# Kernel optimization log

Measured on AMD Instinct MI355X. Metric: run time of the kernel, lower is better.

The kernel has to match this reference:

```python
import jax, jax.numpy as jnp
import numpy as np

EPS = 0.1        # entropic regularization epsilon
MAX_ITER = 15    # fixed number of Sinkhorn iterations (no early stop for determinism)
TINY = 1e-16     # denominator stabilizer, matches torch code
NORM_EPS = 1e-8  # cosine-norm clamp, matches torch code


def setup_inputs() -> dict:
    key = jax.random.key(0)
    k1, k2 = jax.random.split(key)
    x = jax.random.normal(k1, (32, 512, 256), dtype=jnp.float32)
    y = jax.random.normal(k2, (32, 512, 256), dtype=jnp.float32)
    return {"x": x, "y": y}


def _cosine_distance(x, y):
    # C[b,n,m] = 1 - <x_n, y_m> / max(|x_n||y_m|, eps)
    w1 = jnp.linalg.norm(x, axis=-1, keepdims=True)            # [b,n,1]
    w2 = jnp.linalg.norm(y, axis=-1, keepdims=True)            # [b,m,1]
    dots = jnp.einsum('bnd,bmd->bnm', x, y)                    # [b,n,m]
    denom = jnp.maximum(w1 * jnp.swapaxes(w2, -2, -1), NORM_EPS)
    return 1.0 - dots / denom


def _sinkhorn(C):
    nb, n, m = C.shape
    # uniform marginals (a=None, b=None in the torch module); mask is all ones
    a = jnp.full((nb, n), 1.0 / n, dtype=C.dtype)
    b = jnp.full((nb, m), 1.0 / m, dtype=C.dtype)

    def log_K(alpha, beta):
        # log K = (-C + alpha 1^T + 1 beta^T) / eps
        return (-C + alpha[:, :, None] + beta[:, None, :]) / EPS

    def step(carry, _):
        u, v, alpha, beta = carry
        K = jnp.exp(log_K(alpha, beta))
        u = a / (jnp.einsum('bnm,bm->bn', K, v) + TINY)   # K v
        v = b / (jnp.einsum('bnm,bn->bm', K, u) + TINY)   # K^T u
        alpha = alpha + EPS * jnp.log(u)  # absorb u into log scaling
        beta = beta + EPS * jnp.log(v)    # absorb v into log scaling
        return (u, v, alpha, beta), None

    init = (jnp.ones((nb, n), C.dtype), jnp.ones((nb, m), C.dtype),
            jnp.zeros((nb, n), C.dtype), jnp.zeros((nb, m), C.dtype))
    (u, v, alpha, beta), _ = jax.lax.scan(step, init, None, length=MAX_ITER)

    # P = exp(log u + log K + log v) with the FINAL alpha/beta (as in torch code)
    pi = jnp.exp(jnp.log(u)[:, :, None] + log_K(alpha, beta) + jnp.log(v)[:, None, :])
    cost = jnp.sum(pi * C, axis=(-2, -1))  # reduction='none' -> per-batch cost [nb]
    return cost, pi, C


def reference(x, y):
    C = _cosine_distance(x, y)
    return _sinkhorn(C)
```

## Files before the change

### kernel.cpp

```cpp
#include <hip/hip_runtime.h>
#include <hip/hip_fp16.h>
#include <math.h>

#define NB 32
#define NN 512
#define DD 256

constexpr float INV_EPS   = 10.0f;
constexpr float F_TINY    = 1e-16f;
constexpr float F_NORMEPS = 1e-8f;
constexpr float MARG      = 1.0f / 512.0f;

#define BARS_N 2048

typedef __attribute__((ext_vector_type(8))) short bf16x8;
typedef __attribute__((ext_vector_type(4))) float f32x4;

__device__ __forceinline__ unsigned short f2bf(float f) {
    unsigned u = __float_as_uint(f);
    u += 0x7fffu + ((u >> 16) & 1u);
    return (unsigned short)(u >> 16);
}
__device__ __forceinline__ int pack2(float a, float b) {
    return (int)f2bf(a) | ((int)f2bf(b) << 16);
}

__global__ __launch_bounds__(256) void gemm_cos_mfma(
        const float* __restrict__ x, const float* __restrict__ y,
        float* __restrict__ C, float* __restrict__ cost,
        int* __restrict__ bars) {
    int blk = blockIdx.x;
    int b = blk >> 4, ti = (blk >> 2) & 3, tj = blk & 3;
    if (blk == 0) {
        if (threadIdx.x < NB) cost[threadIdx.x] = 0.0f;
        for (int i = threadIdx.x; i < BARS_N; i += 256) bars[i] = 0;
    }
    __shared__ short Ah[128][32], Bh[128][32];
    __shared__ float sNx[128], sNy[128];
    const float* xb = x + ((size_t)b * NN + ti * 128) * DD;
    const float* yb = y + ((size_t)b * NN + tj * 128) * DD;
    int t = threadIdx.x, w = t >> 6, l = t & 63;
    int rw = w * 32, q = l >> 4, low = l & 15;

    f32x4 acc[2][8];
#pragma unroll
    for (int i = 0; i < 2; ++i)
#pragma unroll
        for (int j = 0; j < 8; ++j) acc[i][j] = (f32x4){0.f, 0.f, 0.f, 0.f};

    int sr = t >> 1, h = t & 1;
    int c0i = 2 * h, c1i = 2 * h + 1;
    int sw0 = (c0i ^ ((sr >> 1) & 3)) * 8;
    int sw1 = (c1i ^ ((sr >> 1) & 3)) * 8;
    float ssA = 0.0f, ssB = 0.0f;

    for (int k0 = 0; k0 < DD; k0 += 32) {
        {
            const float4* ga = (const float4*)(xb + (size_t)sr * DD + k0 + 16 * h);
            const float4* gc = (const float4*)(yb + (size_t)sr * DD + k0 + 16 * h);
            float4 a0 = ga[0], a1 = ga[1], a2 = ga[2], a3 = ga[3];
            float4 c0 = gc[0], c1 = gc[1], c2 = gc[2], c3 = gc[3];
            ssA += a0.x*a0.x + a0.y*a0.y + a0.z*a0.z + a0.w*a0.w;
            ssA += a1.x*a1.x + a1.y*a1.y + a1.z*a1.z + a1.w*a1.w;
            ssA += a2.x*a2.x + a2.y*a2.y + a2.z*a2.z + a2.w*a2.w;
            ssA += a3.x*a3.x + a3.y*a3.y + a3.z*a3.z + a3.w*a3.w;
            ssB += c0.x*c0.x + c0.y*c0.y + c0.z*c0.z + c0.w*c0.w;
            ssB += c1.x*c1.x + c1.y*c1.y + c1.z*c1.z + c1.w*c1.w;
            ssB += c2.x*c2.x + c2.y*c2.y + c2.z*c2.z + c2.w*c2.w;
            ssB += c3.x*c3.x + c3.y*c3.y + c3.z*c3.z + c3.w*c3.w;
            int4 pa0 = { pack2(a0.x,a0.y), pack2(a0.z,a0.w),
                         pack2(a1.x,a1.y), pack2(a1.z,a1.w) };
            int4 pa1 = { pack2(a2.x,a2.y), pack2(a2.z,a2.w),
                         pack2(a3.x,a3.y), pack2(a3.z,a3.w) };
            int4 pc0 = { pack2(c0.x,c0.y), pack2(c0.z,c0.w),
                         pack2(c1.x,c1.y), pack2(c1.z,c1.w) };
            int4 pc1 = { pack2(c2.x,c2.y), pack2(c2.z,c2.w),
                         pack2(c3.x,c3.y), pack2(c3.z,c3.w) };
            *(int4*)&Ah[sr][sw0] = pa0; *(int4*)&Ah[sr][sw1] = pa1;
            *(int4*)&Bh[sr][sw0] = pc0; *(int4*)&Bh[sr][sw1] = pc1;
        }
        __syncthreads();

        bf16x8 ah[2];
#pragma unroll
        for (int ti2 = 0; ti2 < 2; ++ti2) {
            int m = rw + ti2 * 16 + low;
            int pq = (q ^ ((m >> 1) & 3)) * 8;
            ah[ti2] = *(const bf16x8*)&Ah[m][pq];
        }
#pragma unroll
        for (int tj2 = 0; tj2 < 8; ++tj2) {
            int n = tj2 * 16 + low;
            int pq = (q ^ ((n >> 1) & 3)) * 8;
            bf16x8 bh = *(const bf16x8*)&Bh[n][pq];
#pragma unroll
            for (int ti2 = 0; ti2 < 2; ++ti2)
                acc[ti2][tj2] = __builtin_amdgcn_mfma_f32_16x16x32_bf16(
                    ah[ti2], bh, acc[ti2][tj2], 0, 0, 0);
        }
        __syncthreads();
    }

    float tA = ssA + __shfl_xor(ssA, 1);
    float tB = ssB + __shfl_xor(ssB, 1);
    if (h == 0) { sNx[sr] = sqrtf(tA); sNy[sr] = sqrtf(tB); }
    __syncthreads();

    float* Cb = C + (size_t)b * NN * NN;
#pragma unroll
    for (int ti2 = 0; ti2 < 2; ++ti2) {
#pragma unroll
        for (int tj2 = 0; tj2 < 8; ++tj2) {
            int ml0 = rw + ti2 * 16 + q * 4;
            int nl  = tj2 * 16 + low;
            int gm0 = ti * 128 + ml0;
            int gn  = tj * 128 + nl;
            float nyc = sNy[nl];
            f32x4 a = acc[ti2][tj2];
#pragma unroll
            for (int reg = 0; reg < 4; ++reg) {
                int gm = gm0 + reg;
                float d = 1.0f - a[reg] / fmaxf(sNx[ml0 + reg] * nyc, F_NORMEPS);
                Cb[(size_t)gm * NN + gn] = d;
            }
        }
    }
}

__global__ __launch_bounds__(512, 2) void sink_fused(
        const float* __restrict__ C,
        float* __restrict__ cp0, float* __restrict__ cp1,
        float* __restrict__ pi, float* __restrict__ cost,
        int* __restrict__ bars) {
    int blk = blockIdx.x;
    int xcd = blk & 7, qq = blk >> 3;
    int o = qq & 7;
    int b = ((qq >> 3) << 3) | xcd;
    int tt = threadIdx.x, w = tt >> 6, l = tt & 63;
    int* flags = &bars[b * 64];

    __shared__ float sW[NN];
    __shared__ float sWP[8][NN];
    __shared__ float sPart[8];

    int4 raw[8];
    {
        const float* Cl = C + ((size_t)b * NN + o * 64 + w * 8) * NN + 8 * l;
#pragma unroll
        for (int i = 0; i < 8; ++i) {
            float4 c0 = *(const float4*)(Cl + (size_t)i * NN);
            float4 c1 = *(const float4*)(Cl + (size_t)i * NN + 4);
            __half h[8];
            h[0] = __float2half(__expf(-INV_EPS * c0.x));
            h[1] = __float2half(__expf(-INV_EPS * c0.y));
            h[2] = __float2half(__expf(-INV_EPS * c0.z));
            h[3] = __float2half(__expf(-INV_EPS * c0.w));
            h[4] = __float2half(__expf(-INV_EPS * c1.x));
            h[5] = __float2half(__expf(-INV_EPS * c1.y));
            h[6] = __float2half(__expf(-INV_EPS * c1.z));
            h[7] = __float2half(__expf(-INV_EPS * c1.w));
            raw[i] = *(const int4*)h;
        }
    }

    float A[8], Pr[8];
#pragma unroll
    for (int i = 0; i < 8; ++i) { A[i] = 1.0f; Pr[i] = 0.0f; }
    float Br = 1.0f;

    float* cpr = cp0;
    float* cpw = cp1;

    for (int t = 1; t <= 15; ++t) {
        if (t == 1) {
            sW[tt] = 1.0f;
        } else {
            if (tt < 8) {
                while (__hip_atomic_load(&flags[tt], __ATOMIC_RELAXED,
                                         __HIP_MEMORY_SCOPE_AGENT) < t - 1)
                    __builtin_amdgcn_s_sleep(1);
            }
            __syncthreads();
            float sv = 0.0f;
#pragma unroll
            for (int k = 0; k < 8; ++k)
                sv += __hip_atomic_load(
                    &cpr[(size_t)(b * 8 + k) * NN + tt],
                    __ATOMIC_RELAXED, __HIP_MEMORY_SCOPE_AGENT);
            float vv = MARG / (Br * sv + F_TINY);
            Br *= vv;
            sW[tt] = Br * vv;
        }
        __syncthreads();

        float wr[8];
        *(float4*)&wr[0] = *(const float4*)&sW[8 * l];
        *(float4*)&wr[4] = *(const float4*)&sW[8 * l + 4];

        float p[8];
#pragma unroll
        for (int e = 0; e < 8; ++e) p[e] = 0.0f;
#pragma unroll
        for (int i = 0; i < 8; ++i) {
            const __half* hv = (const __half*)&raw[i];
            float f0 = __half2float(hv[0]), f1 = __half2float(hv[1]);
            float f2 = __half2float(hv[2]), f3 = __half2float(hv[3]);
            float f4 = __half2float(hv[4]), f5 = __half2float(hv[5]);
            float f6 = __half2float(hv[6]), f7 = __half2float(hv[7]);
            float s = 0.0f;
            s = fmaf(f0, wr[0], s); s = fmaf(f1, wr[1], s);
            s = fmaf(f2, wr[2], s); s = fmaf(f3, wr[3], s);
            s = fmaf(f4, wr[4], s); s = fmaf(f5, wr[5], s);
            s = fmaf(f6, wr[6], s); s = fmaf(f7, wr[7], s);
#pragma unroll
            for (int off = 32; off; off >>= 1) s += __shfl_xor(s, off);
            float uu = MARG / (A[i] * s + F_TINY);
            A[i] *= uu;
            if (t == 15) Pr[i] = A[i] * uu;
            float ai = A[i];
            p[0] = fmaf(f0, ai, p[0]); p[1] = fmaf(f1, ai, p[1]);
            p[2] = fmaf(f2, ai, p[2]); p[3] = fmaf(f3, ai, p[3]);
            p[4] = fmaf(f4, ai, p[4]); p[5] = fmaf(f5, ai, p[5]);
            p[6] = fmaf(f6, ai, p[6]); p[7] = fmaf(f7, ai, p[7]);
        }
        *(float4*)&sWP[w][8 * l]     = make_float4(p[0], p[1], p[2], p[3]);
        *(float4*)&sWP[w][8 * l + 4] = make_float4(p[4], p[5], p[6], p[7]);
        __syncthreads();
        float cs = 0.0f;
#pragma unroll
        for (int ww = 0; ww < 8; ++ww) cs += sWP[ww][tt];
        cpw[(size_t)(b * 8 + o) * NN + tt] = cs;

        __syncthreads();
        if (tt == 0)
            __hip_atomic_store(&flags[o], t, __ATOMIC_RELAXED,
                               __HIP_MEMORY_SCOPE_AGENT);

        float* tmp = cpr; cpr = cpw; cpw = tmp;
    }

    if (tt < 8) {
        while (__hip_atomic_load(&flags[tt], __ATOMIC_RELAXED,
                                 __HIP_MEMORY_SCOPE_AGENT) < 15)
            __builtin_amdgcn_s_sleep(1);
    }
    __syncthreads();
    {
        float sv = 0.0f;
#pragma unroll
        for (int k = 0; k < 8; ++k)
            sv += __hip_atomic_load(
                &cpr[(size_t)(b * 8 + k) * NN + tt],
                __ATOMIC_RELAXED, __HIP_MEMORY_SCOPE_AGENT);
        float vv = MARG / (Br * sv + F_TINY);
        sW[tt] = Br * vv * vv;
    }
    __syncthreads();

    float q0[8];
    *(float4*)&q0[0] = *(const float4*)&sW[4 * l];
    *(float4*)&q0[4] = *(const float4*)&sW[256 + 4 * l];
    const float* Cb = C + (size_t)b * NN * NN;
    float* pib = pi + (size_t)b * NN * NN;
    float csum = 0.0f;
#pragma unroll 2
    for (int i = 0; i < 8; ++i) {
        int r = o * 64 + w * 8 + i;
        float pf = Pr[i];
        const float* crow = Cb + (size_t)r * NN;
        float* prow = pib + (size_t)r * NN;
        float4 c0 = *(const float4*)(crow + 4 * l);
        float4 c1 = *(const float4*)(crow + 256 + 4 * l);
        float pv0 = pf * q0[0] * __expf(-INV_EPS * c0.x);
        float pv1 = pf * q0[1] * __expf(-INV_EPS * c0.y);
        float pv2 = pf * q0[2] * __expf(-INV_EPS * c0.z);
        float pv3 = pf * q0[3] * __expf(-INV_EPS * c0.w);
        float pv4 = pf * q0[4] * __expf(-INV_EPS * c1.x);
        float pv5 = pf * q0[5] * __expf(-INV_EPS * c1.y);
        float pv6 = pf * q0[6] * __expf(-INV_EPS * c1.z);
        float pv7 = pf * q0[7] * __expf(-INV_EPS * c1.w);
        *(float4*)(prow + 4 * l)       = make_float4(pv0, pv1, pv2, pv3);
        *(float4*)(prow + 256 + 4 * l) = make_float4(pv4, pv5, pv6, pv7);
        csum = fmaf(pv0, c0.x, csum); csum = fmaf(pv1, c0.y, csum);
        csum = fmaf(pv2, c0.z, csum); csum = fmaf(pv3, c0.w, csum);
        csum = fmaf(pv4, c1.x, csum); csum = fmaf(pv5, c1.y, csum);
        csum = fmaf(pv6, c1.z, csum); csum = fmaf(pv7, c1.w, csum);
    }
#pragma unroll
    for (int off = 32; off; off >>= 1) csum += __shfl_xor(csum, off);
    if (l == 0) sPart[w] = csum;
    __syncthreads();
    if (tt == 0) {
        float tot = 0.0f;
#pragma unroll
        for (int ww = 0; ww < 8; ++ww) tot += sPart[ww];
        atomicAdd(&cost[b], tot);
    }
}

extern "C" void kernel_launch(void* const* d_in, const int* in_sizes, int n_in,
                              void* d_out, int out_size, void* d_ws, size_t ws_size,
                              hipStream_t stream) {
    const float* x = (const float*)d_in[0];
    const float* y = (const float*)d_in[1];
    float* out  = (float*)d_out;
    float* cost = out;
    float* pi   = out + 32;
    float* C    = out + 32 + (size_t)NB * NN * NN;

    int* bars = (int*)d_ws;
    float* cp0 = (float*)((char*)d_ws + 8192);
    float* cp1 = cp0 + (size_t)NB * 8 * NN;

    gemm_cos_mfma<<<dim3(512), dim3(256), 0, stream>>>(
        x, y, C, cost, bars);

    const float* C_p = C;
    float* cp0_p = cp0; float* cp1_p = cp1;
    float* pi_p = pi; float* cost_p = cost; int* bars_p = bars;
    void* args[] = { &C_p, &cp0_p, &cp1_p, &pi_p, &cost_p, &bars_p };
    hipLaunchCooperativeKernel(reinterpret_cast<void*>(sink_fused),
                               dim3(256), dim3(512), args, 0, stream);
}
```

Baseline: 174.9 us.

## Fuse cosine-distance GEMM into cooperative Sinkhorn kernel, build exp(-C/eps) from LDS

Merges the separate MFMA GEMM kernel into the cooperative Sinkhorn kernel. Each block now computes its own 64x512 strip of C, writes it out, and stores the fp16 exp(-C/eps) tile in shared memory, so the strip no longer has to be read back from global memory. The launch is replaced by two memsets. The trade-off is that each block reloads all of y for its batch (eight times redundant), and shared-memory use grows to about 130 KB at 2 blocks per CU.

```diff
diff --git a/kernel.cpp b/kernel.cpp
--- a/kernel.cpp
+++ b/kernel.cpp
@@ -11,8 +11,6 @@
 constexpr float F_NORMEPS = 1e-8f;
 constexpr float MARG      = 1.0f / 512.0f;
 
-#define BARS_N 2048
-
 typedef __attribute__((ext_vector_type(8))) short bf16x8;
 typedef __attribute__((ext_vector_type(4))) float f32x4;
 
@@ -24,111 +22,13 @@
 __device__ __forceinline__ int pack2(float a, float b) {
     return (int)f2bf(a) | ((int)f2bf(b) << 16);
 }
-
-__global__ __launch_bounds__(256) void gemm_cos_mfma(
+__device__ __forceinline__ float sq4(float4 v) {
+    return v.x * v.x + v.y * v.y + v.z * v.z + v.w * v.w;
+}
+
+__global__ __launch_bounds__(512, 2) void sinkhorn_mega(
         const float* __restrict__ x, const float* __restrict__ y,
-        float* __restrict__ C, float* __restrict__ cost,
-        int* __restrict__ bars) {
-    int blk = blockIdx.x;
-    int b = blk >> 4, ti = (blk >> 2) & 3, tj = blk & 3;
-    if (blk == 0) {
-        if (threadIdx.x < NB) cost[threadIdx.x] = 0.0f;
-        for (int i = threadIdx.x; i < BARS_N; i += 256) bars[i] = 0;
-    }
-    __shared__ short Ah[128][32], Bh[128][32];
-    __shared__ float sNx[128], sNy[128];
-    const float* xb = x + ((size_t)b * NN + ti * 128) * DD;
-    const float* yb = y + ((size_t)b * NN + tj * 128) * DD;
-    int t = threadIdx.x, w = t >> 6, l = t & 63;
-    int rw = w * 32, q = l >> 4, low = l & 15;
-
-    f32x4 acc[2][8];
-#pragma unroll
-    for (int i = 0; i < 2; ++i)
-#pragma unroll
-        for (int j = 0; j < 8; ++j) acc[i][j] = (f32x4){0.f, 0.f, 0.f, 0.f};
-
-    int sr = t >> 1, h = t & 1;
-    int c0i = 2 * h, c1i = 2 * h + 1;
-    int sw0 = (c0i ^ ((sr >> 1) & 3)) * 8;
-    int sw1 = (c1i ^ ((sr >> 1) & 3)) * 8;
-    float ssA = 0.0f, ssB = 0.0f;
-
-    for (int k0 = 0; k0 < DD; k0 += 32) {
-        {
-            const float4* ga = (const float4*)(xb + (size_t)sr * DD + k0 + 16 * h);
-            const float4* gc = (const float4*)(yb + (size_t)sr * DD + k0 + 16 * h);
-            float4 a0 = ga[0], a1 = ga[1], a2 = ga[2], a3 = ga[3];
-            float4 c0 = gc[0], c1 = gc[1], c2 = gc[2], c3 = gc[3];
-            ssA += a0.x*a0.x + a0.y*a0.y + a0.z*a0.z + a0.w*a0.w;
-            ssA += a1.x*a1.x + a1.y*a1.y + a1.z*a1.z + a1.w*a1.w;
-            ssA += a2.x*a2.x + a2.y*a2.y + a2.z*a2.z + a2.w*a2.w;
-            ssA += a3.x*a3.x + a3.y*a3.y + a3.z*a3.z + a3.w*a3.w;
-            ssB += c0.x*c0.x + c0.y*c0.y + c0.z*c0.z + c0.w*c0.w;
-            ssB += c1.x*c1.x + c1.y*c1.y + c1.z*c1.z + c1.w*c1.w;
-            ssB += c2.x*c2.x + c2.y*c2.y + c2.z*c2.z + c2.w*c2.w;
-            ssB += c3.x*c3.x + c3.y*c3.y + c3.z*c3.z + c3.w*c3.w;
-            int4 pa0 = { pack2(a0.x,a0.y), pack2(a0.z,a0.w),
-                         pack2(a1.x,a1.y), pack2(a1.z,a1.w) };
-            int4 pa1 = { pack2(a2.x,a2.y), pack2(a2.z,a2.w),
-                         pack2(a3.x,a3.y), pack2(a3.z,a3.w) };
-            int4 pc0 = { pack2(c0.x,c0.y), pack2(c0.z,c0.w),
-                         pack2(c1.x,c1.y), pack2(c1.z,c1.w) };
-            int4 pc1 = { pack2(c2.x,c2.y), pack2(c2.z,c2.w),
-                         pack2(c3.x,c3.y), pack2(c3.z,c3.w) };
-            *(int4*)&Ah[sr][sw0] = pa0; *(int4*)&Ah[sr][sw1] = pa1;
-            *(int4*)&Bh[sr][sw0] = pc0; *(int4*)&Bh[sr][sw1] = pc1;
-        }
-        __syncthreads();
-
-        bf16x8 ah[2];
-#pragma unroll
-        for (int ti2 = 0; ti2 < 2; ++ti2) {
-            int m = rw + ti2 * 16 + low;
-            int pq = (q ^ ((m >> 1) & 3)) * 8;
-            ah[ti2] = *(const bf16x8*)&Ah[m][pq];
-        }
-#pragma unroll
-        for (int tj2 = 0; tj2 < 8; ++tj2) {
-            int n = tj2 * 16 + low;
-            int pq = (q ^ ((n >> 1) & 3)) * 8;
-            bf16x8 bh = *(const bf16x8*)&Bh[n][pq];
-#pragma unroll
-            for (int ti2 = 0; ti2 < 2; ++ti2)
-                acc[ti2][tj2] = __builtin_amdgcn_mfma_f32_16x16x32_bf16(
-                    ah[ti2], bh, acc[ti2][tj2], 0, 0, 0);
-        }
-        __syncthreads();
-    }
-
-    float tA = ssA + __shfl_xor(ssA, 1);
-    float tB = ssB + __shfl_xor(ssB, 1);
-    if (h == 0) { sNx[sr] = sqrtf(tA); sNy[sr] = sqrtf(tB); }
-    __syncthreads();
-
-    float* Cb = C + (size_t)b * NN * NN;
-#pragma unroll
-    for (int ti2 = 0; ti2 < 2; ++ti2) {
-#pragma unroll
-        for (int tj2 = 0; tj2 < 8; ++tj2) {
-            int ml0 = rw + ti2 * 16 + q * 4;
-            int nl  = tj2 * 16 + low;
-            int gm0 = ti * 128 + ml0;
-            int gn  = tj * 128 + nl;
-            float nyc = sNy[nl];
-            f32x4 a = acc[ti2][tj2];
-#pragma unroll
-            for (int reg = 0; reg < 4; ++reg) {
-                int gm = gm0 + reg;
-                float d = 1.0f - a[reg] / fmaxf(sNx[ml0 + reg] * nyc, F_NORMEPS);
-                Cb[(size_t)gm * NN + gn] = d;
-            }
-        }
-    }
-}
-
-__global__ __launch_bounds__(512, 2) void sink_fused(
-        const float* __restrict__ C,
+        float* __restrict__ C,
         float* __restrict__ cp0, float* __restrict__ cp1,
         float* __restrict__ pi, float* __restrict__ cost,
         int* __restrict__ bars) {
@@ -137,31 +37,117 @@
     int o = qq & 7;
     int b = ((qq >> 3) << 3) | xcd;
     int tt = threadIdx.x, w = tt >> 6, l = tt & 63;
+    int q = l >> 4, low = l & 15;
     int* flags = &bars[b * 64];
 
+    __shared__ short Ah[64][32], Bh[512][32];
+    __shared__ __half sE[64][520];
     __shared__ float sW[NN];
     __shared__ float sWP[8][NN];
+    __shared__ float sNx[64], sNy[512];
     __shared__ float sPart[8];
 
+    const float* xb = x + ((size_t)b * NN + o * 64) * DD;
+    const float* yb = y + (size_t)b * NN * DD;
+
+    f32x4 acc[4][4];
+#pragma unroll
+    for (int m = 0; m < 4; ++m)
+#pragma unroll
+        for (int nj = 0; nj < 4; ++nj) acc[m][nj] = (f32x4){0.f, 0.f, 0.f, 0.f};
+
+    int sbase = (tt >> 1) & 3;
+    float ssA = 0.0f, ssB = 0.0f;
+
+    for (int k0 = 0; k0 < DD; k0 += 32) {
+        {
+            const float4* gy = (const float4*)(yb + (size_t)tt * DD + k0);
+            float4 b0 = gy[0], b1 = gy[1], b2 = gy[2], b3 = gy[3];
+            float4 b4 = gy[4], b5 = gy[5], b6 = gy[6], b7 = gy[7];
+            ssB += sq4(b0) + sq4(b1) + sq4(b2) + sq4(b3)
+                 + sq4(b4) + sq4(b5) + sq4(b6) + sq4(b7);
+            int4 c0 = { pack2(b0.x,b0.y), pack2(b0.z,b0.w),
+                        pack2(b1.x,b1.y), pack2(b1.z,b1.w) };
+            int4 c1 = { pack2(b2.x,b2.y), pack2(b2.z,b2.w),
+                        pack2(b3.x,b3.y), pack2(b3.z,b3.w) };
+            int4 c2 = { pack2(b4.x,b4.y), pack2(b4.z,b4.w),
+                        pack2(b5.x,b5.y), pack2(b5.z,b5.w) };
+            int4 c3 = { pack2(b6.x,b6.y), pack2(b6.z,b6.w),
+                        pack2(b7.x,b7.y), pack2(b7.z,b7.w) };
+            *(int4*)&Bh[tt][(0 ^ sbase) * 8] = c0;
+            *(int4*)&Bh[tt][(1 ^ sbase) * 8] = c1;
+            *(int4*)&Bh[tt][(2 ^ sbase) * 8] = c2;
+            *(int4*)&Bh[tt][(3 ^ sbase) * 8] = c3;
+        }
+        if (tt < 64) {
+            const float4* gx = (const float4*)(xb + (size_t)tt * DD + k0);
+            float4 a0 = gx[0], a1 = gx[1], a2 = gx[2], a3 = gx[3];
+            float4 a4 = gx[4], a5 = gx[5], a6 = gx[6], a7 = gx[7];
+            ssA += sq4(a0) + sq4(a1) + sq4(a2) + sq4(a3)
+                 + sq4(a4) + sq4(a5) + sq4(a6) + sq4(a7);
+            int4 c0 = { pack2(a0.x,a0.y), pack2(a0.z,a0.w),
+                        pack2(a1.x,a1.y), pack2(a1.z,a1.w) };
+            int4 c1 = { pack2(a2.x,a2.y), pack2(a2.z,a2.w),
+                        pack2(a3.x,a3.y), pack2(a3.z,a3.w) };
+            int4 c2 = { pack2(a4.x,a4.y), pack2(a4.z,a4.w),
+                        pack2(a5.x,a5.y), pack2(a5.z,a5.w) };
+            int4 c3 = { pack2(a6.x,a6.y), pack2(a6.z,a6.w),
+                        pack2(a7.x,a7.y), pack2(a7.z,a7.w) };
+            *(int4*)&Ah[tt][(0 ^ sbase) * 8] = c0;
+            *(int4*)&Ah[tt][(1 ^ sbase) * 8] = c1;
+            *(int4*)&Ah[tt][(2 ^ sbase) * 8] = c2;
+            *(int4*)&Ah[tt][(3 ^ sbase) * 8] = c3;
+        }
+        __syncthreads();
+
+        bf16x8 af[4], bf[4];
+#pragma unroll
+        for (int m = 0; m < 4; ++m) {
+            int r = m * 16 + low;
+            af[m] = *(const bf16x8*)&Ah[r][(q ^ ((r >> 1) & 3)) * 8];
+        }
+#pragma unroll
+        for (int nj = 0; nj < 4; ++nj) {
+            int r = w * 64 + nj * 16 + low;
+            bf[nj] = *(const bf16x8*)&Bh[r][(q ^ ((r >> 1) & 3)) * 8];
+        }
+#pragma unroll
+        for (int nj = 0; nj < 4; ++nj)
+#pragma unroll
+            for (int m = 0; m < 4; ++m)
+                acc[m][nj] = __builtin_amdgcn_mfma_f32_16x16x32_bf16(
+                    af[m], bf[nj], acc[m][nj], 0, 0, 0);
+        __syncthreads();
+    }
+
+    if (tt < 64) sNx[tt] = sqrtf(ssA);
+    sNy[tt] = sqrtf(ssB);
+    __syncthreads();
+
+    float* Cb = C + ((size_t)b * NN + o * 64) * NN;
+#pragma unroll
+    for (int m = 0; m < 4; ++m) {
+#pragma unroll
+        for (int nj = 0; nj < 4; ++nj) {
+            int rl0 = m * 16 + q * 4;
+            int cl  = w * 64 + nj * 16 + low;
+            float nyc = sNy[cl];
+            f32x4 a = acc[m][nj];
+#pragma unroll
+            for (int reg = 0; reg < 4; ++reg) {
+                int rl = rl0 + reg;
+                float d = 1.0f - a[reg] / fmaxf(sNx[rl] * nyc, F_NORMEPS);
+                Cb[(size_t)rl * NN + cl] = d;
+                sE[rl][cl] = __float2half(__expf(-INV_EPS * d));
+            }
+        }
+    }
+    __syncthreads();
+
     int4 raw[8];
-    {
-        const float* Cl = C + ((size_t)b * NN + o * 64 + w * 8) * NN + 8 * l;
-#pragma unroll
-        for (int i = 0; i < 8; ++i) {
-            float4 c0 = *(const float4*)(Cl + (size_t)i * NN);
-            float4 c1 = *(const float4*)(Cl + (size_t)i * NN + 4);
-            __half h[8];
-            h[0] = __float2half(__expf(-INV_EPS * c0.x));
-            h[1] = __float2half(__expf(-INV_EPS * c0.y));
-            h[2] = __float2half(__expf(-INV_EPS * c0.z));
-            h[3] = __float2half(__expf(-INV_EPS * c0.w));
-            h[4] = __float2half(__expf(-INV_EPS * c1.x));
-            h[5] = __float2half(__expf(-INV_EPS * c1.y));
-            h[6] = __float2half(__expf(-INV_EPS * c1.z));
-            h[7] = __float2half(__expf(-INV_EPS * c1.w));
-            raw[i] = *(const int4*)h;
-        }
-    }
+#pragma unroll
+    for (int i = 0; i < 8; ++i)
+        raw[i] = *(const int4*)&sE[w * 8 + i][8 * l];
 
     float A[8], Pr[8];
 #pragma unroll
@@ -260,14 +246,14 @@
     float q0[8];
     *(float4*)&q0[0] = *(const float4*)&sW[4 * l];
     *(float4*)&q0[4] = *(const float4*)&sW[256 + 4 * l];
-    const float* Cb = C + (size_t)b * NN * NN;
+    const float* Cb2 = C + (size_t)b * NN * NN;
     float* pib = pi + (size_t)b * NN * NN;
     float csum = 0.0f;
 #pragma unroll 2
     for (int i = 0; i < 8; ++i) {
         int r = o * 64 + w * 8 + i;
         float pf = Pr[i];
-        const float* crow = Cb + (size_t)r * NN;
+        const float* crow = Cb2 + (size_t)r * NN;
         float* prow = pib + (size_t)r * NN;
         float4 c0 = *(const float4*)(crow + 4 * l);
         float4 c1 = *(const float4*)(crow + 256 + 4 * l);
@@ -312,13 +298,14 @@
     float* cp0 = (float*)((char*)d_ws + 8192);
     float* cp1 = cp0 + (size_t)NB * 8 * NN;
 
-    gemm_cos_mfma<<<dim3(512), dim3(256), 0, stream>>>(
-        x, y, C, cost, bars);
-
-    const float* C_p = C;
+    hipMemsetAsync(bars, 0, 8192, stream);
+    hipMemsetAsync(cost, 0, NB * sizeof(float), stream);
+
+    const float* x_p = x; const float* y_p = y; float* C_p = C;
     float* cp0_p = cp0; float* cp1_p = cp1;
     float* pi_p = pi; float* cost_p = cost; int* bars_p = bars;
-    void* args[] = { &C_p, &cp0_p, &cp1_p, &pi_p, &cost_p, &bars_p };
-    hipLaunchCooperativeKernel(reinterpret_cast<void*>(sink_fused),
+    void* args[] = { &x_p, &y_p, &C_p, &cp0_p, &cp1_p,
+                     &pi_p, &cost_p, &bars_p };
+    hipLaunchCooperativeKernel(reinterpret_cast<void*>(sinkhorn_mega),
                                dim3(256), dim3(512), args, 0, stream);
 }
```

Result: slower. 198.5 us (+13.5%).
